# Performance work log

Hardware: AMD Instinct MI355X
Metric: run time of the kernel (lower is better)

The kernel has to match this reference:

```python
import jax, jax.numpy as jnp
import numpy as np

B, S, D_IN, HID, H = 4, 2048, 1024, 1024, 16
DH = HID // H


def setup_inputs() -> dict:
    key = jax.random.key(0)
    ks = jax.random.split(key, 10)
    s = 0.02
    return {
        "x": jax.random.normal(ks[0], (B, S, D_IN), dtype=jnp.float32),
        "Wq": jax.random.normal(ks[1], (D_IN, HID), dtype=jnp.float32) * s,
        "bq": jnp.zeros((HID,), dtype=jnp.float32),
        "Wk": jax.random.normal(ks[2], (D_IN, HID), dtype=jnp.float32) * s,
        "bk": jnp.zeros((HID,), dtype=jnp.float32),
        "Wv": jax.random.normal(ks[3], (D_IN, HID), dtype=jnp.float32) * s,
        "bv": jnp.zeros((HID,), dtype=jnp.float32),
        "Wo": jax.random.normal(ks[4], (HID, HID), dtype=jnp.float32) * s,
        "bo": jnp.zeros((HID,), dtype=jnp.float32),
        "padding_mask": jax.random.randint(ks[5], (B, S), 0, 2, dtype=jnp.int32),
    }


def reference(x, Wq, bq, Wk, bk, Wv, bv, Wo, bo, padding_mask):
    b, s, _ = x.shape
    q = (x @ Wq + bq).reshape(b, s, H, DH)  # [b, s, h, dh]
    k = (x @ Wk + bk).reshape(b, s, H, DH)
    v = (x @ Wv + bv).reshape(b, s, H, DH)

    # ALiBi: symmetric |i-j| distance bias, per-head slopes 2^{-m}
    r = jnp.arange(s)
    pos = jnp.abs(r[None, :] - r[:, None]).astype(jnp.float32)  # [s, s]
    step = 8.0 / H
    slopes = jnp.power(2.0, -jnp.arange(step, 8.0 + step, step, dtype=jnp.float32))  # [h]
    alibi = slopes[:, None, None] * pos[None, :, :]  # [h, s, s]

    scale = jnp.sqrt(jnp.float32(DH))
    attn = jnp.einsum("bqhd,bkhd->bhqk", q, k)
    attn = (attn - alibi[None]) / scale
    attn = jnp.where(padding_mask[:, None, None, :] == 0, -jnp.inf, attn)
    p = jax.nn.softmax(attn, axis=-1)

    out = jnp.einsum("bhqk,bkhd->bqhd", p, v).reshape(b, s, HID)
    return out @ Wo + bo
```

## Files before the change

### kernel.cpp

```cpp
#include <hip/hip_runtime.h>
#include <stdint.h>

#define NB     4
#define SEQ    2048
#define NH     16
#define DHD    64
#define DM     1024
#define MTOT   (NB*SEQ)

typedef __attribute__((ext_vector_type(8))) short bf16x8;
typedef __attribute__((ext_vector_type(4))) float f32x4;

__device__ __forceinline__ short f2bf(float f) {
  uint32_t u = __float_as_uint(f);
  u = (u + 0x7FFFu + ((u >> 16) & 1u)) >> 16;
  return (short)u;
}

__device__ __forceinline__ uint32_t cvtpk(float lo, float hi) {
  uint32_t r;
  asm("v_cvt_pk_bf16_f32 %0, %1, %2" : "=v"(r) : "v"(lo), "v"(hi));
  return r;
}

__device__ __forceinline__ f32x4 mfma16(bf16x8 a, bf16x8 b, f32x4 c) {
  return __builtin_amdgcn_mfma_f32_16x16x32_bf16(a, b, c, 0, 0, 0);
}

__device__ __forceinline__ void async16(const void* g, void* l) {
  __builtin_amdgcn_global_load_lds(
      (const __attribute__((address_space(1))) void*)g,
      (__attribute__((address_space(3))) void*)l, 16, 0, 0);
}

__global__ void k_cast(const float* __restrict__ in, short* __restrict__ out, int n) {
  int i = (blockIdx.x * blockDim.x + threadIdx.x) * 8;
  if (i >= n) return;
  float4 a = *reinterpret_cast<const float4*>(in + i);
  float4 b = *reinterpret_cast<const float4*>(in + i + 4);
  bf16x8 v;
  v[0] = f2bf(a.x); v[1] = f2bf(a.y); v[2] = f2bf(a.z); v[3] = f2bf(a.w);
  v[4] = f2bf(b.x); v[5] = f2bf(b.y); v[6] = f2bf(b.z); v[7] = f2bf(b.w);
  *reinterpret_cast<bf16x8*>(out + i) = v;
}

__global__ void k_maskbias(const int* __restrict__ pm, float* __restrict__ fb, int n) {
  int i = blockIdx.x * blockDim.x + threadIdx.x;
  if (i < n) fb[i] = pm[i] ? 0.0f : -1e30f;
}

__global__ void k_transpose(const float* __restrict__ in, short* __restrict__ out) {
  __shared__ float tile[32][33];
  int n0 = blockIdx.x * 32, k0 = blockIdx.y * 32;
  int tx = threadIdx.x, ty = threadIdx.y;
  #pragma unroll
  for (int i = 0; i < 32; i += 8)
    tile[ty + i][tx] = in[(size_t)(k0 + ty + i) * DM + n0 + tx];
  __syncthreads();
  #pragma unroll
  for (int i = 0; i < 32; i += 8)
    out[(size_t)(n0 + ty + i) * DM + k0 + tx] = f2bf(tile[tx][ty + i]);
}

template<int MODE>
__global__ void __launch_bounds__(256) k_gemm(const short* __restrict__ A,
                                              const short* __restrict__ Bt,
                                              const float* __restrict__ bias,
                                              void* __restrict__ Cv, float scale) {
  __shared__ short lA[128 * 32];
  __shared__ short lB[128 * 32];
  int m0 = blockIdx.x * 128, n0 = blockIdx.y * 128;
  int tid = threadIdx.x, lane = tid & 63, w = tid >> 6;
  int wr = w >> 1, wc = w & 1;
  int l15 = lane & 15, lg = lane >> 4;
  f32x4 acc[4][4] = {};

  int r0 = tid >> 2, c0 = (tid & 3) * 8;
  int r1 = (tid + 256) >> 2, c1 = ((tid + 256) & 3) * 8;
  const short* ga0 = A + (size_t)(m0 + r0) * DM + c0;
  const short* ga1 = A + (size_t)(m0 + r1) * DM + c1;
  const short* gb0 = Bt + (size_t)(n0 + r0) * DM + c0;
  const short* gb1 = Bt + (size_t)(n0 + r1) * DM + c1;
  short* lA0 = lA + w * 512;
  short* lA1 = lA + 2048 + w * 512;
  short* lB0 = lB + w * 512;
  short* lB1 = lB + 2048 + w * 512;

  for (int k0 = 0; k0 < DM; k0 += 32) {
    async16(ga0 + k0, lA0);
    async16(ga1 + k0, lA1);
    async16(gb0 + k0, lB0);
    async16(gb1 + k0, lB1);
    __syncthreads();
    bf16x8 af[4], bfr[4];
    #pragma unroll
    for (int i = 0; i < 4; ++i) {
      af[i]  = *reinterpret_cast<const bf16x8*>(lA + (wr * 64 + i * 16 + l15) * 32 + lg * 8);
      bfr[i] = *reinterpret_cast<const bf16x8*>(lB + (wc * 64 + i * 16 + l15) * 32 + lg * 8);
    }
    #pragma unroll
    for (int i = 0; i < 4; ++i)
      #pragma unroll
      for (int j = 0; j < 4; ++j)
        acc[i][j] = mfma16(af[i], bfr[j], acc[i][j]);
    __syncthreads();
  }

  #pragma unroll
  for (int j = 0; j < 4; ++j) {
    int cg = n0 + wc * 64 + j * 16 + l15;
    float bv = bias[cg];
    #pragma unroll
    for (int i = 0; i < 4; ++i) {
      #pragma unroll
      for (int r = 0; r < 4; ++r) {
        int rg = m0 + wr * 64 + i * 16 + lg * 4 + r;
        float val = (acc[i][j][r] + bv) * scale;
        if (MODE == 0)
          ((short*)Cv)[(size_t)rg * DM + cg] = f2bf(val);
        else if (MODE == 1)
          ((short*)Cv)[((size_t)((rg >> 11) * DM + cg)) * SEQ + (rg & 2047)] = f2bf(val);
        else
          ((float*)Cv)[(size_t)rg * DM + cg] = val;
      }
    }
  }
}

__global__ void __launch_bounds__(256) k_attn(const short* __restrict__ Q,
                                              const short* __restrict__ Kb,
                                              const short* __restrict__ Vt,
                                              const float* __restrict__ fbias,
                                              short* __restrict__ O) {
  __shared__ short lK[64 * 64];
  __shared__ short lV[64 * 64];
  __shared__ uint32_t pbuf[4 * 16 * 36];
  int qt = blockIdx.x, bh = blockIdx.y;
  int b = bh >> 4, h = bh & 15;
  int tid = threadIdx.x, lane = tid & 63, w = tid >> 6;
  int l15 = lane & 15, lg = lane >> 4;
  int q0 = qt * 64 + w * 16;
  float c2 = exp2f(-0.5f * (float)(h + 1)) * 0.125f;

  const short* qp = Q + (size_t)(b * SEQ + q0 + l15) * DM + h * DHD + lg * 8;
  bf16x8 bq0 = *reinterpret_cast<const bf16x8*>(qp);
  bf16x8 bq1 = *reinterpret_cast<const bf16x8*>(qp + 32);

  int srow0 = w * 8 + (lane >> 3);
  int srow1 = srow0 + 32;
  int sc0 = (lane & 7) ^ (srow0 & 7);
  int sc1 = (lane & 7) ^ (srow1 & 7);
  const short* kg0 = Kb + (size_t)(b * SEQ + srow0) * DM + h * DHD + sc0 * 8;
  const short* kg1 = Kb + (size_t)(b * SEQ + srow1) * DM + h * DHD + sc1 * 8;
  const short* vg0 = Vt + ((size_t)bh * DHD + srow0) * SEQ + sc0 * 8;
  const short* vg1 = Vt + ((size_t)bh * DHD + srow1) * SEQ + sc1 * 8;
  short* dK0 = lK + w * 512;
  short* dK1 = lK + 2048 + w * 512;
  short* dV0 = lV + w * 512;
  short* dV1 = lV + 2048 + w * 512;

  const float* fb = fbias + b * SEQ;
  uint32_t* wb = pbuf + w * 576 + l15 * 36;

  float mrun = -1e30f, ssum = 0.0f;
  f32x4 acc[4] = {};
  float d0 = (float)(q0 + l15) - (float)(lg * 4);

  for (int kt = 0; kt < SEQ; kt += 64) {
    async16(kg0, dK0);
    async16(kg1, dK1);
    async16(vg0, dV0);
    async16(vg1, dV1);
    kg0 += (size_t)64 * DM; kg1 += (size_t)64 * DM; vg0 += 64; vg1 += 64;

    float4 fb4[4];
    #pragma unroll
    for (int t = 0; t < 4; ++t)
      fb4[t] = *reinterpret_cast<const float4*>(fb + kt + t * 16 + lg * 4);

    __syncthreads();

    f32x4 st[4];
    #pragma unroll
    for (int t = 0; t < 4; ++t) {
      int row = t * 16 + l15, sw = row & 7;
      bf16x8 k0 = *reinterpret_cast<const bf16x8*>(lK + row * 64 + (lg ^ sw) * 8);
      bf16x8 k1 = *reinterpret_cast<const bf16x8*>(lK + row * 64 + ((lg + 4) ^ sw) * 8);
      f32x4 z = {};
      z = mfma16(k0, bq0, z);
      st[t] = mfma16(k1, bq1, z);
    }

    float l[4][4];
    #pragma unroll
    for (int t = 0; t < 4; ++t) {
      l[t][0] = fmaf(-c2, fabsf(d0 - (float)(t * 16 + 0)), st[t][0] + fb4[t].x);
      l[t][1] = fmaf(-c2, fabsf(d0 - (float)(t * 16 + 1)), st[t][1] + fb4[t].y);
      l[t][2] = fmaf(-c2, fabsf(d0 - (float)(t * 16 + 2)), st[t][2] + fb4[t].z);
      l[t][3] = fmaf(-c2, fabsf(d0 - (float)(t * 16 + 3)), st[t][3] + fb4[t].w);
    }

    float tmax = l[0][0];
    #pragma unroll
    for (int t = 0; t < 4; ++t)
      #pragma unroll
      for (int r = 0; r < 4; ++r)
        tmax = fmaxf(tmax, l[t][r]);
    tmax = fmaxf(tmax, __shfl_xor(tmax, 16));
    tmax = fmaxf(tmax, __shfl_xor(tmax, 32));

    float mn = fmaxf(mrun, tmax);
    float fsc = __expf(mrun - mn);
    mrun = mn;

    float rs = 0.0f;
    #pragma unroll
    for (int t = 0; t < 4; ++t)
      #pragma unroll
      for (int r = 0; r < 4; ++r) {
        float p = __expf(l[t][r] - mn);
        l[t][r] = p;
        rs += p;
      }
    rs += __shfl_xor(rs, 16);
    rs += __shfl_xor(rs, 32);
    ssum = ssum * fsc + rs;
    #pragma unroll
    for (int td = 0; td < 4; ++td) acc[td] *= fsc;

    #pragma unroll
    for (int t = 0; t < 4; ++t) {
      uint2 wv = { cvtpk(l[t][0], l[t][1]), cvtpk(l[t][2], l[t][3]) };
      *reinterpret_cast<uint2*>(wb + t * 8 + lg * 2) = wv;
    }
    asm volatile("s_waitcnt lgkmcnt(0)" ::: "memory");
    __builtin_amdgcn_sched_barrier(0);

    #pragma unroll
    for (int ks = 0; ks < 2; ++ks) {
      int t = ks * 2 + (lg >> 1);
      bf16x8 pf = *reinterpret_cast<const bf16x8*>(wb + t * 8 + (lg & 1) * 4);
      #pragma unroll
      for (int td = 0; td < 4; ++td) {
        int row = td * 16 + l15, sw = row & 7;
        bf16x8 vf = *reinterpret_cast<const bf16x8*>(lV + row * 64 + ((ks * 4 + lg) ^ sw) * 8);
        acc[td] = mfma16(vf, pf, acc[td]);
      }
    }
    d0 -= 64.0f;
    __syncthreads();
  }

  float inv = 1.0f / ssum;
  short* op = O + (size_t)(b * SEQ + q0 + l15) * DM + h * DHD;
  #pragma unroll
  for (int td = 0; td < 4; ++td) {
    uint2 wv = { cvtpk(acc[td][0] * inv, acc[td][1] * inv),
                 cvtpk(acc[td][2] * inv, acc[td][3] * inv) };
    *reinterpret_cast<uint2*>(op + td * 16 + lg * 4) = wv;
  }
}

extern "C" void kernel_launch(void* const* d_in, const int* in_sizes, int n_in,
                              void* d_out, int out_size, void* d_ws, size_t ws_size,
                              hipStream_t stream) {
  const float* x  = (const float*)d_in[0];
  const float* Wq = (const float*)d_in[1];
  const float* bq = (const float*)d_in[2];
  const float* Wk = (const float*)d_in[3];
  const float* bk = (const float*)d_in[4];
  const float* Wv = (const float*)d_in[5];
  const float* bv = (const float*)d_in[6];
  const float* Wo = (const float*)d_in[7];
  const float* bo = (const float*)d_in[8];
  const int*   pm = (const int*)d_in[9];

  char* ws = (char*)d_ws;
  const size_t MB = 1ull << 20;
  short* xb  = (short*)(ws + 0 * MB);
  short* q   = (short*)(ws + 16 * MB);
  short* k   = (short*)(ws + 32 * MB);
  short* vt  = (short*)(ws + 48 * MB);
  short* ob  = (short*)(ws + 64 * MB);
  short* wqt = (short*)(ws + 80 * MB);
  short* wkt = (short*)(ws + 82 * MB);
  short* wvt = (short*)(ws + 84 * MB);
  short* wot = (short*)(ws + 86 * MB);
  float* fbias = (float*)(ws + 88 * MB);

  k_cast<<<dim3(MTOT * DM / 8 / 256), dim3(256), 0, stream>>>(x, xb, MTOT * DM);
  k_maskbias<<<dim3(MTOT / 256), dim3(256), 0, stream>>>(pm, fbias, MTOT);
  k_transpose<<<dim3(32, 32), dim3(32, 8), 0, stream>>>(Wq, wqt);
  k_transpose<<<dim3(32, 32), dim3(32, 8), 0, stream>>>(Wk, wkt);
  k_transpose<<<dim3(32, 32), dim3(32, 8), 0, stream>>>(Wv, wvt);
  k_transpose<<<dim3(32, 32), dim3(32, 8), 0, stream>>>(Wo, wot);
  k_gemm<0><<<dim3(64, 8), dim3(256), 0, stream>>>(xb, wqt, bq, q, 0.125f);
  k_gemm<0><<<dim3(64, 8), dim3(256), 0, stream>>>(xb, wkt, bk, k, 1.0f);
  k_gemm<1><<<dim3(64, 8), dim3(256), 0, stream>>>(xb, wvt, bv, vt, 1.0f);
  k_attn<<<dim3(SEQ / 64, NB * NH), dim3(256), 0, stream>>>(q, k, vt, fbias, ob);
  k_gemm<2><<<dim3(64, 8), dim3(256), 0, stream>>>(ob, wot, bo, d_out, 1.0f);
}
```

Measured before the change: 272.8 us.

## Double-buffer K/V tiles in attention, use exp2 softmax with lazy rescale, swizzle GEMM grid

The attention kernel now keeps two LDS buffers for K and V and prefetches the next tile while computing on the current one, so there is one barrier per iteration and load latency is hidden. Softmax is moved to base 2: log2(e) is folded into the Q scale and the ALiBi slope, and raw v_exp_f32 is used. The running max is only rescaled when some lane's new max exceeds the old one by more than 8. MFMA sections are wrapped in setprio, max and sum use tree reductions, and the GEMM block index is remapped to improve L2 reuse. This uses twice the LDS and relies on the lazy-rescale threshold staying within fp32 range. The mask bias presumably still holds -inf or a large negative value, which still works when scaled in base 2.

```diff
diff --git a/kernel.cpp b/kernel.cpp
--- a/kernel.cpp
+++ b/kernel.cpp
@@ -21,6 +21,16 @@
   uint32_t r;
   asm("v_cvt_pk_bf16_f32 %0, %1, %2" : "=v"(r) : "v"(lo), "v"(hi));
   return r;
+}
+
+__device__ __forceinline__ float exp2a(float x) {
+  float r;
+  asm("v_exp_f32 %0, %1" : "=v"(r) : "v"(x));
+  return r;
+}
+
+__device__ __forceinline__ float max3f(float a, float b, float c) {
+  return fmaxf(fmaxf(a, b), c);
 }
 
 __device__ __forceinline__ f32x4 mfma16(bf16x8 a, bf16x8 b, f32x4 c) {
@@ -69,7 +79,9 @@
                                               void* __restrict__ Cv, float scale) {
   __shared__ short lA[128 * 32];
   __shared__ short lB[128 * 32];
-  int m0 = blockIdx.x * 128, n0 = blockIdx.y * 128;
+  int lin = blockIdx.y * gridDim.x + blockIdx.x;
+  int s = ((lin & 7) << 6) | (lin >> 3);
+  int m0 = (s & 63) * 128, n0 = (s >> 6) * 128;
   int tid = threadIdx.x, lane = tid & 63, w = tid >> 6;
   int wr = w >> 1, wc = w & 1;
   int l15 = lane & 15, lg = lane >> 4;
@@ -132,15 +144,15 @@
                                               const short* __restrict__ Vt,
                                               const float* __restrict__ fbias,
                                               short* __restrict__ O) {
-  __shared__ short lK[64 * 64];
-  __shared__ short lV[64 * 64];
+  __shared__ short lK[2][64 * 64];
+  __shared__ short lV[2][64 * 64];
   __shared__ uint32_t pbuf[4 * 16 * 36];
   int qt = blockIdx.x, bh = blockIdx.y;
   int b = bh >> 4, h = bh & 15;
   int tid = threadIdx.x, lane = tid & 63, w = tid >> 6;
   int l15 = lane & 15, lg = lane >> 4;
   int q0 = qt * 64 + w * 16;
-  float c2 = exp2f(-0.5f * (float)(h + 1)) * 0.125f;
+  float c2 = exp2f(-0.5f * (float)(h + 1)) * 0.125f * 1.44269504f;
 
   const short* qp = Q + (size_t)(b * SEQ + q0 + l15) * DM + h * DHD + lg * 8;
   bf16x8 bq0 = *reinterpret_cast<const bf16x8*>(qp);
@@ -154,42 +166,57 @@
   const short* kg1 = Kb + (size_t)(b * SEQ + srow1) * DM + h * DHD + sc1 * 8;
   const short* vg0 = Vt + ((size_t)bh * DHD + srow0) * SEQ + sc0 * 8;
   const short* vg1 = Vt + ((size_t)bh * DHD + srow1) * SEQ + sc1 * 8;
-  short* dK0 = lK + w * 512;
-  short* dK1 = lK + 2048 + w * 512;
-  short* dV0 = lV + w * 512;
-  short* dV1 = lV + 2048 + w * 512;
 
   const float* fb = fbias + b * SEQ;
   uint32_t* wb = pbuf + w * 576 + l15 * 36;
+  int sw = l15 & 7;
 
   float mrun = -1e30f, ssum = 0.0f;
   f32x4 acc[4] = {};
   float d0 = (float)(q0 + l15) - (float)(lg * 4);
 
+  async16(kg0, &lK[0][w * 512]);
+  async16(kg1, &lK[0][2048 + w * 512]);
+  async16(vg0, &lV[0][w * 512]);
+  async16(vg1, &lV[0][2048 + w * 512]);
+  kg0 += (size_t)64 * DM; kg1 += (size_t)64 * DM; vg0 += 64; vg1 += 64;
+  asm volatile("s_waitcnt vmcnt(0)" ::: "memory");
+  __builtin_amdgcn_s_barrier();
+  __builtin_amdgcn_sched_barrier(0);
+
   for (int kt = 0; kt < SEQ; kt += 64) {
-    async16(kg0, dK0);
-    async16(kg1, dK1);
-    async16(vg0, dV0);
-    async16(vg1, dV1);
-    kg0 += (size_t)64 * DM; kg1 += (size_t)64 * DM; vg0 += 64; vg1 += 64;
+    int cur = (kt >> 6) & 1;
+    const short* Kc = lK[cur];
+    const short* Vc = lV[cur];
 
     float4 fb4[4];
     #pragma unroll
     for (int t = 0; t < 4; ++t)
       fb4[t] = *reinterpret_cast<const float4*>(fb + kt + t * 16 + lg * 4);
-
-    __syncthreads();
+    __builtin_amdgcn_sched_barrier(0);
+
+    if (kt + 64 < SEQ) {
+      short* nK = (short*)lK[cur ^ 1];
+      short* nV = (short*)lV[cur ^ 1];
+      async16(kg0, nK + w * 512);
+      async16(kg1, nK + 2048 + w * 512);
+      async16(vg0, nV + w * 512);
+      async16(vg1, nV + 2048 + w * 512);
+      kg0 += (size_t)64 * DM; kg1 += (size_t)64 * DM; vg0 += 64; vg1 += 64;
+    }
 
     f32x4 st[4];
+    __builtin_amdgcn_s_setprio(1);
     #pragma unroll
     for (int t = 0; t < 4; ++t) {
-      int row = t * 16 + l15, sw = row & 7;
-      bf16x8 k0 = *reinterpret_cast<const bf16x8*>(lK + row * 64 + (lg ^ sw) * 8);
-      bf16x8 k1 = *reinterpret_cast<const bf16x8*>(lK + row * 64 + ((lg + 4) ^ sw) * 8);
+      int row = t * 16 + l15;
+      bf16x8 k0 = *reinterpret_cast<const bf16x8*>(Kc + row * 64 + (lg ^ sw) * 8);
+      bf16x8 k1 = *reinterpret_cast<const bf16x8*>(Kc + row * 64 + ((lg + 4) ^ sw) * 8);
       f32x4 z = {};
       z = mfma16(k0, bq0, z);
       st[t] = mfma16(k1, bq1, z);
     }
+    __builtin_amdgcn_s_setprio(0);
 
     float l[4][4];
     #pragma unroll
@@ -200,55 +227,64 @@
       l[t][3] = fmaf(-c2, fabsf(d0 - (float)(t * 16 + 3)), st[t][3] + fb4[t].w);
     }
 
-    float tmax = l[0][0];
-    #pragma unroll
-    for (int t = 0; t < 4; ++t)
-      #pragma unroll
-      for (int r = 0; r < 4; ++r)
-        tmax = fmaxf(tmax, l[t][r]);
+    float ma = max3f(l[0][0], l[0][1], l[0][2]);
+    float mb = max3f(l[0][3], l[1][0], l[1][1]);
+    float mc = max3f(l[1][2], l[1][3], l[2][0]);
+    float md = max3f(l[2][1], l[2][2], l[2][3]);
+    float me = max3f(l[3][0], l[3][1], l[3][2]);
+    float tmax = fmaxf(max3f(ma, mb, mc), max3f(md, me, l[3][3]));
     tmax = fmaxf(tmax, __shfl_xor(tmax, 16));
     tmax = fmaxf(tmax, __shfl_xor(tmax, 32));
 
-    float mn = fmaxf(mrun, tmax);
-    float fsc = __expf(mrun - mn);
-    mrun = mn;
-
-    float rs = 0.0f;
+    if (!__all(tmax <= mrun + 8.0f)) {
+      float mn = fmaxf(mrun, tmax);
+      float fsc = exp2a(mrun - mn);
+      mrun = mn;
+      ssum *= fsc;
+      #pragma unroll
+      for (int td = 0; td < 4; ++td) acc[td] *= fsc;
+    }
+
+    float p[16];
     #pragma unroll
     for (int t = 0; t < 4; ++t)
       #pragma unroll
-      for (int r = 0; r < 4; ++r) {
-        float p = __expf(l[t][r] - mn);
-        l[t][r] = p;
-        rs += p;
-      }
+      for (int r = 0; r < 4; ++r)
+        p[t * 4 + r] = exp2a(l[t][r] - mrun);
+    float a0 = p[0] + p[1],  a1 = p[2] + p[3],  a2 = p[4] + p[5],  a3 = p[6] + p[7];
+    float a4 = p[8] + p[9],  a5 = p[10] + p[11], a6 = p[12] + p[13], a7 = p[14] + p[15];
+    float b0 = a0 + a1, b1 = a2 + a3, b2 = a4 + a5, b3 = a6 + a7;
+    float rs = (b0 + b1) + (b2 + b3);
     rs += __shfl_xor(rs, 16);
     rs += __shfl_xor(rs, 32);
-    ssum = ssum * fsc + rs;
-    #pragma unroll
-    for (int td = 0; td < 4; ++td) acc[td] *= fsc;
+    ssum += rs;
 
     #pragma unroll
     for (int t = 0; t < 4; ++t) {
-      uint2 wv = { cvtpk(l[t][0], l[t][1]), cvtpk(l[t][2], l[t][3]) };
+      uint2 wv = { cvtpk(p[t * 4 + 0], p[t * 4 + 1]), cvtpk(p[t * 4 + 2], p[t * 4 + 3]) };
       *reinterpret_cast<uint2*>(wb + t * 8 + lg * 2) = wv;
     }
     asm volatile("s_waitcnt lgkmcnt(0)" ::: "memory");
     __builtin_amdgcn_sched_barrier(0);
 
+    __builtin_amdgcn_s_setprio(1);
     #pragma unroll
     for (int ks = 0; ks < 2; ++ks) {
       int t = ks * 2 + (lg >> 1);
       bf16x8 pf = *reinterpret_cast<const bf16x8*>(wb + t * 8 + (lg & 1) * 4);
       #pragma unroll
       for (int td = 0; td < 4; ++td) {
-        int row = td * 16 + l15, sw = row & 7;
-        bf16x8 vf = *reinterpret_cast<const bf16x8*>(lV + row * 64 + ((ks * 4 + lg) ^ sw) * 8);
+        int row = td * 16 + l15;
+        bf16x8 vf = *reinterpret_cast<const bf16x8*>(Vc + row * 64 + ((ks * 4 + lg) ^ sw) * 8);
         acc[td] = mfma16(vf, pf, acc[td]);
       }
     }
+    __builtin_amdgcn_s_setprio(0);
     d0 -= 64.0f;
-    __syncthreads();
+
+    asm volatile("s_waitcnt vmcnt(0)" ::: "memory");
+    __builtin_amdgcn_s_barrier();
+    __builtin_amdgcn_sched_barrier(0);
   }
 
   float inv = 1.0f / ssum;
@@ -294,7 +330,7 @@
   k_transpose<<<dim3(32, 32), dim3(32, 8), 0, stream>>>(Wk, wkt);
   k_transpose<<<dim3(32, 32), dim3(32, 8), 0, stream>>>(Wv, wvt);
   k_transpose<<<dim3(32, 32), dim3(32, 8), 0, stream>>>(Wo, wot);
-  k_gemm<0><<<dim3(64, 8), dim3(256), 0, stream>>>(xb, wqt, bq, q, 0.125f);
+  k_gemm<0><<<dim3(64, 8), dim3(256), 0, stream>>>(xb, wqt, bq, q, 0.125f * 1.44269504f);
   k_gemm<0><<<dim3(64, 8), dim3(256), 0, stream>>>(xb, wkt, bk, k, 1.0f);
   k_gemm<1><<<dim3(64, 8), dim3(256), 0, stream>>>(xb, wvt, bv, vt, 1.0f);
   k_attn<<<dim3(SEQ / 64, NB * NH), dim3(256), 0, stream>>>(q, k, vt, fbias, ob);
```

New measurement: 295.2 us. 8.2% more time.
